# Performance work log

Measured on AMD Instinct MI355X. Metric: run time of the kernel, lower is better.

## Reference

```python
import math
import jax, jax.numpy as jnp
import numpy as np

_GELU_C = math.sqrt(2.0 / math.pi)

def _gelu_tanh(x):
    return 0.5 * x * (1.0 + jnp.tanh(_GELU_C * (x + 0.044715 * x * x * x)))

def _l2_normalize(v, eps=1e-12):
    # matches F.normalize: v / max(||v||, eps)
    n = jnp.sqrt(jnp.sum(v * v, axis=-1, keepdims=True))
    return v / jnp.maximum(n, eps)

def setup_inputs() -> dict:
    key = jax.random.key(0)
    k1, k2, k3 = jax.random.split(key, 3)
    B, T, D = 8, 2048, 1024
    x = jax.random.normal(k1, (B, T, D), dtype=jnp.float32)
    # nn.Parameter initial values from the module
    log_alpha = jnp.asarray(math.log(math.exp(0.5) - 1.0), dtype=jnp.float32)
    log_sigma = jnp.asarray(math.log(1.0), dtype=jnp.float32)
    return {"x": x, "log_alpha": log_alpha, "log_sigma": log_sigma}

def reference(x, log_alpha, log_sigma):
    B, T, D = x.shape
    alpha = jax.nn.softplus(log_alpha)
    sigma = jax.nn.softplus(log_sigma)
    scale = 1.0 / math.sqrt(D)
    # full strictly-past causal attention (triu with diagonal=0 masks self too)
    sim = jnp.einsum('btd,bsd->bts', x, x) * scale            # [B,T,T]
    causal = jnp.triu(jnp.ones((T, T), dtype=bool), k=0)      # True = masked
    sim = jnp.where(causal[None], -jnp.inf, sim)
    # NaN-safe masked softmax: fully-masked rows (t=0) -> all zeros,
    # matching torch softmax + nan_to_num(nan=0.0)
    m = jnp.max(sim, axis=-1, keepdims=True)
    m_safe = jnp.where(jnp.isfinite(m), m, 0.0)
    e = jnp.exp(sim - m_safe)                                 # -inf -> 0
    denom = jnp.sum(e, axis=-1, keepdims=True)
    attn = jnp.where(denom > 0, e / jnp.where(denom > 0, denom, 1.0), 0.0)
    context = jnp.einsum('bts,bsd->btd', attn, x)             # [B,T,D]
    cos_sim = jnp.sum(_l2_normalize(x) * _l2_normalize(context), axis=-1)  # [B,T]
    novelty = jnp.clip(1.0 - cos_sim, 0.0, 2.0) / 2.0
    novelty = jnp.nan_to_num(novelty, nan=1.0)
    gate = 1.0 + alpha * jnp.tanh(sigma * novelty[..., None])
    return _gelu_tanh(x * gate)
```

## Files before the change

### kernel.cpp

```cpp
#include <hip/hip_runtime.h>
#include <math.h>

#define TN 2048
#define DN 1024

typedef __attribute__((ext_vector_type(8))) _Float16 half8;
typedef __attribute__((ext_vector_type(4))) _Float16 half4v;
typedef __attribute__((ext_vector_type(4))) float f32x4;

__device__ __forceinline__ f32x4 mfma16(half8 a, half8 b, f32x4 c) {
  return __builtin_amdgcn_mfma_f32_16x16x32_f16(a, b, c, 0, 0, 0);
}

#define BAR_LDS()  asm volatile("s_waitcnt lgkmcnt(0)\ns_barrier" ::: "memory")
#define WAITVM0()  asm volatile("s_waitcnt vmcnt(0)" ::: "memory")

__device__ __forceinline__ int img_off(int key, int f) {
  const int kg = key >> 2;
  const int p  = ((kg & 1) << 2) | (kg >> 1);
  return (f >> 4) * 512 + p * 64 + (key & 3) * 16 + (f & 15);
}

__global__ __launch_bounds__(256) void convert_x(const float* __restrict__ x,
                                                 _Float16* __restrict__ w) {
  const long long gid = (long long)blockIdx.x * 256 + threadIdx.x;
  const long long e   = gid * 8;
  const int bt   = (int)(e >> 15);
  const int et   = (int)(e & 32767);
  const int f16b = et >> 9;
  const int p    = (et >> 6) & 7;
  const int row  = (et >> 4) & 3;
  const int col0 = et & 15;
  const int kg   = ((p & 3) << 1) | (p >> 2);
  const int key  = kg * 4 + row;
  const size_t xoff = ((size_t)bt * 32 + key) * DN + f16b * 16 + col0;
  float4 u0 = *(const float4*)(x + xoff);
  float4 u1 = *(const float4*)(x + xoff + 4);
  half8 h = {(_Float16)u0.x, (_Float16)u0.y, (_Float16)u0.z, (_Float16)u0.w,
             (_Float16)u1.x, (_Float16)u1.y, (_Float16)u1.z, (_Float16)u1.w};
  *(half8*)(w + e) = h;
}

#define ISSUE4(T, O0, O1, O2, O3)                                             \
  asm volatile("ds_read_b64_tr_b16 %0, %4 offset:" O0 "\n\t"                  \
               "ds_read_b64_tr_b16 %1, %4 offset:" O1 "\n\t"                  \
               "ds_read_b64_tr_b16 %2, %4 offset:" O2 "\n\t"                  \
               "ds_read_b64_tr_b16 %3, %4 offset:" O3                         \
               : "=&v"(T[0]), "=&v"(T[1]), "=&v"(T[2]), "=&v"(T[3])           \
               : "v"(ab));

#define MFMA2(T, CT0, CT1)                                                    \
  {                                                                           \
    half8 bf0 = __builtin_shufflevector(T[0], T[1], 0, 1, 2, 3, 4, 5, 6, 7);  \
    half8 bf1 = __builtin_shufflevector(T[2], T[3], 0, 1, 2, 3, 4, 5, 6, 7);  \
    oacc[CT0] = mfma16(aP, bf0, oacc[CT0]);                                   \
    oacc[CT1] = mfma16(aP, bf1, oacc[CT1]);                                   \
  }

template <bool WS>
__global__ __launch_bounds__(512, 4)
void attn_gate(const float* __restrict__ x, const _Float16* __restrict__ wsx,
               const float* __restrict__ pla, const float* __restrict__ pls,
               float* __restrict__ out) {
  __shared__ _Float16 Kbuf[32768];
  __shared__ _Float16 Sred[8][16][44];
  __shared__ float l_s[16], gate_s[16];

  const int tid = threadIdx.x;
  const int w   = tid >> 6;
  const int l   = tid & 63;
  const int lr  = l & 15;
  const int lg  = l >> 4;
  const int kq  = w;

  const int b   = blockIdx.x & 7;
  const int q16 = 127 - (blockIdx.x >> 3);
  const int qbase = q16 * 16;
  const int nkt   = (qbase + 14) / 32 + 1;

  const float alpha = log1pf(expf(pla[0]));
  const float sigma = log1pf(expf(pls[0]));

  const float* xb = x + (size_t)b * TN * DN;
  float*       ob = out + (size_t)b * TN * DN;

  const int kg0 = lr >> 2;
  const int bk0 = ((((kg0 & 1) << 2) | (kg0 >> 1)) << 6) + (lr & 3) * 16 + (lg & 1) * 8;
  const int kg1 = 4 + (lr >> 2);
  const int bk1 = ((((kg1 & 1) << 2) | (kg1 >> 1)) << 6) + (lr & 3) * 16 + (lg & 1) * 8;

  auto STAGE = [&](int t) {
    if constexpr (WS) {
      const _Float16* tn = wsx + (size_t)(b * 64 + t) * 32768;
#pragma unroll
      for (int i = 0; i < 8; ++i)
        __builtin_amdgcn_global_load_lds(
            (const __attribute__((address_space(1))) void*)(tn + w * 4096 + i * 512 + l * 8),
            (__attribute__((address_space(3))) void*)(&Kbuf[w * 4096 + i * 512]), 16, 0, 0);
    } else {
      const int skey = tid >> 4, sc = tid & 15;
      const float* kp = xb + (size_t)(t * 32 + skey) * DN + sc * 4;
#pragma unroll
      for (int j = 0; j < 16; ++j) {
        const int f = sc * 4 + 64 * j;
        float4 v = *(const float4*)(kp + 64 * j);
        half4v h = {(_Float16)v.x, (_Float16)v.y, (_Float16)v.z, (_Float16)v.w};
        *(half4v*)&Kbuf[img_off(skey, f)] = h;
      }
    }
  };

  STAGE(0);

  half8 qf[4];
  if constexpr (WS) {
    const _Float16* qtile = wsx + (size_t)(b * 64 + (q16 >> 1)) * 32768;
    const int qrow = (q16 & 1) * 16 + lr;
    const int g0   = qrow >> 2;
    const int qp   = (((g0 & 1) << 2) | (g0 >> 1)) * 64 + (qrow & 3) * 16 + (lg & 1) * 8;
#pragma unroll
    for (int s = 0; s < 4; ++s)
      qf[s] = *(const half8*)&qtile[(kq * 8 + s * 2 + (lg >> 1)) * 512 + qp];
  } else {
#pragma unroll
    for (int s = 0; s < 4; ++s) {
      const float* qp = xb + (size_t)(qbase + lr) * DN + kq * 128 + s * 32 + lg * 8;
      float4 a = ((const float4*)qp)[0];
      float4 c = ((const float4*)qp)[1];
      half8 h;
      h[0]=(_Float16)a.x; h[1]=(_Float16)a.y; h[2]=(_Float16)a.z; h[3]=(_Float16)a.w;
      h[4]=(_Float16)c.x; h[5]=(_Float16)c.y; h[6]=(_Float16)c.z; h[7]=(_Float16)c.w;
      qf[s] = h;
    }
  }

  f32x4 oacc[8];
#pragma unroll
  for (int ct = 0; ct < 8; ++ct) oacc[ct] = f32x4{0.f, 0.f, 0.f, 0.f};
  float l0 = 0.0f;

  if constexpr (!WS) __syncthreads();

  for (int t = 0; t < nkt; ++t) {
    if constexpr (WS) WAITVM0();

    {
      f32x4 sA = f32x4{0.f,0.f,0.f,0.f};
      f32x4 sB = f32x4{0.f,0.f,0.f,0.f};
#pragma unroll
      for (int s = 0; s < 4; ++s) {
        const int base = (kq * 8 + s * 2 + (lg >> 1)) * 512;
        half8 bf0 = *(const half8*)&Kbuf[base + bk0];
        half8 bf1 = *(const half8*)&Kbuf[base + bk1];
        sA = mfma16(bf0, qf[s], sA);
        sB = mfma16(bf1, qf[s], sB);
      }
      half4v hA = {(_Float16)sA[0], (_Float16)sA[1], (_Float16)sA[2], (_Float16)sA[3]};
      half4v hB = {(_Float16)sB[0], (_Float16)sB[1], (_Float16)sB[2], (_Float16)sB[3]};
      *(half4v*)&Sred[kq][lr][lg * 4]      = hA;
      *(half4v*)&Sred[kq][lr][16 + lg * 4] = hB;
    }
    BAR_LDS();

    {
      half8 r0 = *(const half8*)&Sred[0][lr][lg * 8];
      half8 r1 = *(const half8*)&Sred[1][lr][lg * 8];
      half8 r2 = *(const half8*)&Sred[2][lr][lg * 8];
      half8 r3 = *(const half8*)&Sred[3][lr][lg * 8];
      half8 r4 = *(const half8*)&Sred[4][lr][lg * 8];
      half8 r5 = *(const half8*)&Sred[5][lr][lg * 8];
      half8 r6 = *(const half8*)&Sred[6][lr][lg * 8];
      half8 r7 = *(const half8*)&Sred[7][lr][lg * 8];
      half8 sum = ((r0 + r1) + (r2 + r3)) + ((r4 + r5) + (r6 + r7));

      const bool mt = (t == nkt - 1);
      const int  gb = 32 * t + lg * 8;
      half8 aP;
#pragma unroll
      for (int j = 0; j < 8; ++j) {
        float p = __expf((float)sum[j] * 0.03125f);
        if (mt && (gb + j >= qbase + lr)) p = 0.0f;
        l0 += p;
        aP[j] = (_Float16)p;
      }

      const uint32_t ab = (uint32_t)(uintptr_t)(void*)&Kbuf[w * 4096 + l * 4];
      asm volatile("s_waitcnt lgkmcnt(0)" ::: "memory");
      __builtin_amdgcn_sched_barrier(0);
      half4v t0[4], t1[4];
      ISSUE4(t0, "0", "512", "1024", "1536");
      ISSUE4(t1, "2048", "2560", "3072", "3584");
      asm volatile("s_waitcnt lgkmcnt(4)" ::: "memory");
      __builtin_amdgcn_sched_barrier(0);
      MFMA2(t0, 0, 1);
      ISSUE4(t0, "4096", "4608", "5120", "5632");
      asm volatile("s_waitcnt lgkmcnt(4)" ::: "memory");
      __builtin_amdgcn_sched_barrier(0);
      MFMA2(t1, 2, 3);
      ISSUE4(t1, "6144", "6656", "7168", "7680");
      asm volatile("s_waitcnt lgkmcnt(4)" ::: "memory");
      __builtin_amdgcn_sched_barrier(0);
      MFMA2(t0, 4, 5);
      asm volatile("s_waitcnt lgkmcnt(0)" ::: "memory");
      __builtin_amdgcn_sched_barrier(0);
      MFMA2(t1, 6, 7);
    }

    if (t + 1 < nkt) {
      if constexpr (!WS) __syncthreads();
      STAGE(t + 1);
    }
    BAR_LDS();
  }

  {
    float lt = l0 + __shfl_xor(l0, 16);
    lt += __shfl_xor(lt, 32);
    if (w == 0 && lg == 0) l_s[lr] = lt;
  }

  {
    float* ered = (float*)&Sred[0][0][0];
#pragma unroll
    for (int j = 0; j < 4; ++j) {
      const int row = lg * 4 + j;
      const float* xr = xb + (size_t)(qbase + row) * DN + w * 128 + lr;
      float a1 = 0.f, a2 = 0.f, a3 = 0.f;
#pragma unroll
      for (int ct = 0; ct < 8; ++ct) {
        const float xv = xr[ct * 16];
        const float ov = oacc[ct][j];
        a1 += xv * ov; a2 += xv * xv; a3 += ov * ov;
      }
#pragma unroll
      for (int d = 1; d < 16; d <<= 1) {
        a1 += __shfl_xor(a1, d);
        a2 += __shfl_xor(a2, d);
        a3 += __shfl_xor(a3, d);
      }
      if (lr == 0) {
        float* e = ered + (row * 8 + w) * 4;
        e[0] = a1; e[1] = a2; e[2] = a3;
      }
    }
  }
  __syncthreads();
  if (tid < 16) {
    const float* ered = (const float*)&Sred[0][0][0];
    float SxO = 0.f, Sxx = 0.f, SOO = 0.f;
#pragma unroll
    for (int wv = 0; wv < 8; ++wv) {
      const float* e = ered + (tid * 8 + wv) * 4;
      SxO += e[0]; Sxx += e[1]; SOO += e[2];
    }
    const float lden = l_s[tid];
    float cosv = 0.0f;
    if (lden > 0.0f) {
      const float nx = fmaxf(sqrtf(Sxx), 1e-12f);
      const float nc = fmaxf(sqrtf(SOO) / lden, 1e-12f);
      cosv = (SxO / lden) / (nx * nc);
    }
    float nov = fminf(fmaxf(1.0f - cosv, 0.0f), 2.0f) * 0.5f;
    gate_s[tid] = 1.0f + alpha * tanhf(sigma * nov);
  }
  __syncthreads();
  {
#pragma unroll
    for (int j = 0; j < 4; ++j) {
      const int row = lg * 4 + j;
      const float g = gate_s[row];
      const float* xr = xb + (size_t)(qbase + row) * DN + w * 128 + lr;
      float* orow     = ob + (size_t)(qbase + row) * DN + w * 128 + lr;
#pragma unroll
      for (int ct = 0; ct < 8; ++ct) {
        const float z = xr[ct * 16] * g;
        const float u = 0.7978845608028654f * (z + 0.044715f * z * z * z);
        orow[ct * 16] = 0.5f * z * (1.0f + tanhf(u));
      }
    }
  }
}

extern "C" void kernel_launch(void* const* d_in, const int* in_sizes, int n_in,
                              void* d_out, int out_size, void* d_ws, size_t ws_size,
                              hipStream_t stream) {
  const float* x  = (const float*)d_in[0];
  const float* la = (const float*)d_in[1];
  const float* ls = (const float*)d_in[2];
  float* out = (float*)d_out;
  const size_t need = (size_t)8 * 64 * 32768 * 2;
  if (ws_size >= need) {
    convert_x<<<dim3(8192), dim3(256), 0, stream>>>(x, (_Float16*)d_ws);
    attn_gate<true><<<dim3(1024), dim3(512), 0, stream>>>(
        x, (const _Float16*)d_ws, la, ls, out);
  } else {
    attn_gate<false><<<dim3(1024), dim3(512), 0, stream>>>(
        x, (const _Float16*)nullptr, la, ls, out);
  }
}
```

Before: 194.3 us.

## Double-buffer score reduction buffer and hoist transposed K reads before reduction

The per-wave score partials buffer becomes double-buffered by iteration parity. This lets the end-of-iteration LDS barrier be dropped: only a __syncthreads after staging remains in the non-WS path, and in the WS path no barrier is left. The first transposed-K LDS reads are now issued before the partial-score reduction, so their latency overlaps the reduction and exp work. The padding on the score buffer is removed and the small scalar arrays are aliased into it. Risks are LDS bank conflicts from the unpadded rows and a possible race between staging the next K tile and other waves still reading the current one.

Result: slower. 213.0 us (+9.6%).

```diff
diff --git a/kernel.cpp b/kernel.cpp
--- a/kernel.cpp
+++ b/kernel.cpp
@@ -63,8 +63,10 @@
                const float* __restrict__ pla, const float* __restrict__ pls,
                float* __restrict__ out) {
   __shared__ _Float16 Kbuf[32768];
-  __shared__ _Float16 Sred[8][16][44];
-  __shared__ float l_s[16], gate_s[16];
+  __shared__ _Float16 SredD[2][8][16][32];
+  float* l_s    = (float*)&SredD[0][0][0][0];
+  float* gate_s = l_s + 16;
+  float* ered   = gate_s + 16;
 
   const int tid = threadIdx.x;
   const int w   = tid >> 6;
@@ -157,21 +159,26 @@
       }
       half4v hA = {(_Float16)sA[0], (_Float16)sA[1], (_Float16)sA[2], (_Float16)sA[3]};
       half4v hB = {(_Float16)sB[0], (_Float16)sB[1], (_Float16)sB[2], (_Float16)sB[3]};
-      *(half4v*)&Sred[kq][lr][lg * 4]      = hA;
-      *(half4v*)&Sred[kq][lr][16 + lg * 4] = hB;
+      *(half4v*)&SredD[t & 1][kq][lr][lg * 4]      = hA;
+      *(half4v*)&SredD[t & 1][kq][lr][16 + lg * 4] = hB;
     }
     BAR_LDS();
 
     {
-      half8 r0 = *(const half8*)&Sred[0][lr][lg * 8];
-      half8 r1 = *(const half8*)&Sred[1][lr][lg * 8];
-      half8 r2 = *(const half8*)&Sred[2][lr][lg * 8];
-      half8 r3 = *(const half8*)&Sred[3][lr][lg * 8];
-      half8 r4 = *(const half8*)&Sred[4][lr][lg * 8];
-      half8 r5 = *(const half8*)&Sred[5][lr][lg * 8];
-      half8 r6 = *(const half8*)&Sred[6][lr][lg * 8];
-      half8 r7 = *(const half8*)&Sred[7][lr][lg * 8];
-      half8 sum = ((r0 + r1) + (r2 + r3)) + ((r4 + r5) + (r6 + r7));
+      const uint32_t ab = (uint32_t)(uintptr_t)(void*)&Kbuf[w * 4096 + l * 4];
+      half4v t0[4], t1[4];
+      ISSUE4(t0, "0", "512", "1024", "1536");
+      ISSUE4(t1, "2048", "2560", "3072", "3584");
+
+      const _Float16* sp = &SredD[t & 1][0][lr][lg * 8];
+      half8 sum = *(const half8*)(sp);
+      sum = sum + *(const half8*)(sp + 512);
+      sum = sum + *(const half8*)(sp + 1024);
+      sum = sum + *(const half8*)(sp + 1536);
+      sum = sum + *(const half8*)(sp + 2048);
+      sum = sum + *(const half8*)(sp + 2560);
+      sum = sum + *(const half8*)(sp + 3072);
+      sum = sum + *(const half8*)(sp + 3584);
 
       const bool mt = (t == nkt - 1);
       const int  gb = 32 * t + lg * 8;
@@ -184,13 +191,6 @@
         aP[j] = (_Float16)p;
       }
 
-      const uint32_t ab = (uint32_t)(uintptr_t)(void*)&Kbuf[w * 4096 + l * 4];
-      asm volatile("s_waitcnt lgkmcnt(0)" ::: "memory");
-      __builtin_amdgcn_sched_barrier(0);
-      half4v t0[4], t1[4];
-      ISSUE4(t0, "0", "512", "1024", "1536");
-      ISSUE4(t1, "2048", "2560", "3072", "3584");
-      asm volatile("s_waitcnt lgkmcnt(4)" ::: "memory");
       __builtin_amdgcn_sched_barrier(0);
       MFMA2(t0, 0, 1);
       ISSUE4(t0, "4096", "4608", "5120", "5632");
@@ -209,9 +209,11 @@
     if (t + 1 < nkt) {
       if constexpr (!WS) __syncthreads();
       STAGE(t + 1);
-    }
-    BAR_LDS();
-  }
+      if constexpr (!WS) __syncthreads();
+    }
+  }
+
+  BAR_LDS();
 
   {
     float lt = l0 + __shfl_xor(l0, 16);
@@ -220,7 +222,6 @@
   }
 
   {
-    float* ered = (float*)&Sred[0][0][0];
 #pragma unroll
     for (int j = 0; j < 4; ++j) {
       const int row = lg * 4 + j;
@@ -246,7 +247,6 @@
   }
   __syncthreads();
   if (tid < 16) {
-    const float* ered = (const float*)&Sred[0][0][0];
     float SxO = 0.f, Sxx = 0.f, SOO = 0.f;
 #pragma unroll
     for (int wv = 0; wv < 8; ++wv) {
```
